# Optimization experiments

Measured on AMD Instinct MI355X. Metric: run time of the kernel, lower is better.

The kernel has to match this reference:

```python
import jax, jax.numpy as jnp
import numpy as np

B, I, H, T = 64, 128, 256, 1024


def setup_inputs() -> dict:
    key = jax.random.key(0)
    ks = jax.random.split(key, 18)
    stdv = 1.0 / np.sqrt(H)  # reset_parameters: uniform(-1/sqrt(hidden), 1/sqrt(hidden))
    u = lambda k, shape: jax.random.uniform(k, shape, jnp.float32, -stdv, stdv)
    return dict(
        X=jax.random.normal(ks[0], (B, I, T), jnp.float32),
        Mask=jax.random.randint(ks[1], (B, I, T), 0, 2).astype(jnp.float32),
        Delta=jax.random.uniform(ks[2], (B, I, T), jnp.float32),
        x_mean=jnp.float32(0.0),
        Wdgx=u(ks[3], (I, I)), bdgx=u(ks[4], (I,)),
        Wdgh=u(ks[5], (H, I)), bdgh=u(ks[6], (H,)),
        Wxz=u(ks[7], (H, I)), Whz=u(ks[8], (H, H)), Wmz=u(ks[9], (H, I)), bmz=u(ks[10], (H,)),
        Wxr=u(ks[11], (H, I)), Whr=u(ks[12], (H, H)), Wmr=u(ks[13], (H, I)),
        Wxh=u(ks[14], (H, I)), Whh=u(ks[15], (H, H)), Wmh=u(ks[16], (H, I)), bmh=u(ks[17], (H,)),
    )


def _grud(X, Mask, Delta, x_mean, Wdgx, bdgx, Wdgh, bdgh, Wxz, Whz, Wmz, bmz,
          Wxr, Whr, Wmr, Wxh, Whh, Wmh, bmh):
    # [B, I, T] -> time-major [T, B, I] for scan
    Xt = jnp.transpose(X, (2, 0, 1))
    Mt = jnp.transpose(Mask, (2, 0, 1))
    Dt = jnp.transpose(Delta, (2, 0, 1))

    def step(carry, xs):
        h, x_last = carry            # h: [B, H], x_last: [B, I]
        x, m, d = xs                 # each [B, I]
        gamma_x = jnp.exp(-jax.nn.relu(d @ Wdgx.T + bdgx))   # [B, I]
        gamma_h = jnp.exp(-jax.nn.relu(d @ Wdgh.T + bdgh))   # [B, H]
        x_last = jnp.where(m > 0, x, x_last)
        # faithful double imputation as in the torch source
        x1 = m * x + (1 - m) * (gamma_x * x + (1 - gamma_x) * x_mean)
        x2 = m * x1 + (1 - m) * (gamma_x * x_last + (1 - gamma_x) * x_mean)
        hd = gamma_h * h
        z = jax.nn.sigmoid(x2 @ Wxz.T + hd @ Whz.T + m @ Wmz.T + bmz)
        r = jax.nn.sigmoid(x2 @ Wxr.T + hd @ Whr.T + m @ Wmr.T)
        h_tilde = jnp.tanh(x2 @ Wxh.T + (r * hd) @ Whh.T + m @ Wmh.T + bmh)
        h_new = (1 - z) * hd + z * h_tilde
        return (h_new, x_last), h_new

    h0 = jnp.zeros((X.shape[0], Whz.shape[0]), X.dtype)      # Hidden_State buffer (zeros)
    xl0 = jnp.zeros((X.shape[0], X.shape[1]), X.dtype)       # X_last_obs buffer (zeros)
    _, hs = jax.lax.scan(step, (h0, xl0), (Xt, Mt, Dt))      # hs: [T, B, H]
    return jnp.transpose(hs, (1, 0, 2))                      # [B, T, H]


def reference(X, Mask, Delta, x_mean, Wdgx, bdgx, Wdgh, bdgh, Wxz, Whz, Wmz, bmz,
              Wxr, Whr, Wmr, Wxh, Whh, Wmh, bmh):
    return _grud(X, Mask, Delta, x_mean, Wdgx, bdgx, Wdgh, bdgh, Wxz, Whz, Wmz, bmz,
                 Wxr, Whr, Wmr, Wxh, Whh, Wmh, bmh)
```

## Files before the change

### kernel.cpp

```cpp
#include <hip/hip_runtime.h>
#include <cstdint>
#include <cstddef>

typedef _Float16 f16;
typedef _Float16 f16x8 __attribute__((ext_vector_type(8)));
typedef _Float16 f16x2 __attribute__((ext_vector_type(2)));
typedef float f32x4 __attribute__((ext_vector_type(4)));

#define B_ 64
#define I_ 128
#define H_ 256
#define T_ 1024
#define BT_ (B_*T_)

__device__ __forceinline__ uint32_t pack2_f16(float a, float b) {
  union { f16 h; uint16_t u; } ua, ub;
  ua.h = (f16)a; ub.h = (f16)b;
  return ((uint32_t)ub.u << 16) | (uint32_t)ua.u;
}

__device__ __forceinline__ float fdot2_u(uint32_t w, uint32_t x, float acc) {
  union { uint32_t u; f16x2 h; } uw, ux;
  uw.u = w; ux.u = x;
  return __builtin_amdgcn_fdot2(uw.h, ux.h, acc, false);
}

__device__ __forceinline__ float tanh_stable(float s) {
  float a = fabsf(s);
  float e = __expf(-2.f * a);
  float t = (1.f - e) * __fdividef(1.f, 1.f + e);
  return s < 0.f ? -t : t;
}

__device__ __forceinline__ float sigmoidf(float s) {
  return __fdividef(1.f, 1.f + __expf(-s));
}

__device__ __forceinline__ f16x8 load_frag(const f16* row, int k0, int g4) {
  union { uint32_t u[4]; f16x8 h; } r;
  const uint32_t* p0 = (const uint32_t*)(row + k0 + g4);
  const uint32_t* p1 = (const uint32_t*)(row + k0 + 16 + g4);
  r.u[0] = p0[0]; r.u[1] = p0[1];
  r.u[2] = p1[0]; r.u[3] = p1[1];
  return r.h;
}

__global__ void k_transpose_d(const float* __restrict__ D, f16* __restrict__ Dt) {
  __shared__ float tile[64][65];
  int t0 = blockIdx.x * 64, i0 = blockIdx.y * 64, b = blockIdx.z;
  int tx = threadIdx.x, ty = threadIdx.y;
  #pragma unroll
  for (int r = 0; r < 16; ++r) {
    int il = ty + r * 4;
    tile[il][tx] = D[((size_t)(b * I_ + i0 + il)) * T_ + t0 + tx];
  }
  __syncthreads();
  #pragma unroll
  for (int r = 0; r < 16; ++r) {
    int tl = ty + r * 4;
    Dt[((size_t)(b * T_ + t0 + tl)) * I_ + i0 + tx] = (f16)tile[tx][tl];
  }
}

__global__ void k_prep(const float* __restrict__ Wdgx, const float* __restrict__ bdgx,
                       const float* __restrict__ Wdgh, const float* __restrict__ bdgh,
                       const float* __restrict__ Wxz, const float* __restrict__ Whz,
                       const float* __restrict__ Wmz, const float* __restrict__ bmz,
                       const float* __restrict__ Wxr, const float* __restrict__ Whr,
                       const float* __restrict__ Wmr,
                       const float* __restrict__ Wxh, const float* __restrict__ Whh,
                       const float* __restrict__ Wmh, const float* __restrict__ bmh,
                       f16* __restrict__ Wg, float* __restrict__ bg,
                       f16* __restrict__ W3, float* __restrict__ b3,
                       uint32_t* __restrict__ blobR, uint32_t* __restrict__ blobHrg,
                       uint32_t* __restrict__ blobZ4, uint32_t* __restrict__ blobHl4) {
  int tid = blockIdx.x * blockDim.x + threadIdx.x;
  int nth = gridDim.x * blockDim.x;
  for (int idx = tid; idx < 384 * 128; idx += nth) {
    int j = idx >> 7, k = idx & 127;
    float v = (j < 128) ? Wdgx[j * 128 + k] : Wdgh[(j - 128) * 128 + k];
    Wg[idx] = (f16)v;
  }
  for (int j = tid; j < 384; j += nth) bg[j] = (j < 128) ? bdgx[j] : bdgh[j - 128];
  for (int idx = tid; idx < 768 * 256; idx += nth) {
    int j = idx >> 8, c = idx & 255;
    const float* Wx = (j < 256) ? Wxz : ((j < 512) ? Wxr : Wxh);
    const float* Wm = (j < 256) ? Wmz : ((j < 512) ? Wmr : Wmh);
    int jj = j & 255;
    float v = (c < 128) ? Wx[jj * 128 + c] : Wm[jj * 128 + (c - 128)];
    W3[idx] = (f16)v;
  }
  for (int j = tid; j < 768; j += nth)
    b3[j] = (j < 256) ? bmz[j] : ((j < 512) ? 0.0f : bmh[j - 512]);
  for (int idx = tid; idx < 64 * 512; idx += nth) {
    int c = idx >> 9, t = idx & 511;
    int rr = c >> 5, cc = c & 31;
    int ks = t >> 7, rg = t & 127;
    int row = rg * 2 + rr;
    int k = ks * 64 + cc * 2;
    blobR[idx] = pack2_f16(Whr[row * 256 + k], Whr[row * 256 + k + 1]);
  }
  for (int idx = tid; idx < 56 * 512; idx += nth) {
    int c = idx >> 9, t = idx & 511;
    int rr = (c >= 28) ? 1 : 0, cc = c - rr * 28;
    int ks = t >> 7, rg = t & 127;
    int row = rg * 2 + rr;
    int k = ks * 64 + cc * 2;
    blobHrg[idx] = pack2_f16(Whh[row * 256 + k], Whh[row * 256 + k + 1]);
  }
  for (int idx = tid; idx < 16 * 512 * 4; idx += nth) {
    int q = idx & 3, r = idx >> 2;
    int t = r & 511, c4 = r >> 9;
    int rr = c4 >> 3, qq = c4 & 7;
    int ks = t >> 7, rg = t & 127;
    int row = rg * 2 + rr;
    int k = ks * 64 + qq * 8 + q * 2;
    blobZ4[idx] = pack2_f16(Whz[row * 256 + k], Whz[row * 256 + k + 1]);
  }
  for (int idx = tid; idx < 2 * 512 * 4; idx += nth) {
    int q = idx & 3, r = idx >> 2;
    int t = r & 511, rr = r >> 9;
    int ks = t >> 7, rg = t & 127;
    int row = rg * 2 + rr;
    int k = ks * 64 + 56 + q * 2;
    blobHl4[idx] = pack2_f16(Whh[row * 256 + k], Whh[row * 256 + k + 1]);
  }
}

__global__ __launch_bounds__(256) void k_gemm1(const f16* __restrict__ A,
                                               const f16* __restrict__ W,
                                               const float* __restrict__ bias,
                                               float* __restrict__ Gx,
                                               f16* __restrict__ Gh) {
  __shared__ __align__(16) f16 As[64][136];
  __shared__ __align__(16) f16 Ws[128][136];
  int m0 = blockIdx.x * 64, n0 = blockIdx.y * 128;
  int tid = threadIdx.x;
  {
    int r = tid >> 2, sgm = tid & 3;
    const uint4* src = (const uint4*)(A + (size_t)(m0 + r) * 128 + sgm * 32);
    uint4* dst = (uint4*)(&As[r][sgm * 32]);
    #pragma unroll
    for (int q = 0; q < 4; ++q) dst[q] = src[q];
  }
  {
    int r = tid >> 1, hf = tid & 1;
    const uint4* src = (const uint4*)(W + (size_t)(n0 + r) * 128 + hf * 64);
    uint4* dst = (uint4*)(&Ws[r][hf * 64]);
    #pragma unroll
    for (int q = 0; q < 8; ++q) dst[q] = src[q];
  }
  __syncthreads();
  int w = tid >> 6, l = tid & 63;
  int lr = l & 15, g4 = (l >> 4) * 4;
  f32x4 acc[8] = {};
  #pragma unroll
  for (int kk = 0; kk < 4; ++kk) {
    int k0 = kk * 32;
    f16x8 a = load_frag(&As[w * 16 + lr][0], k0, g4);
    #pragma unroll
    for (int nt = 0; nt < 8; ++nt) {
      f16x8 bf = load_frag(&Ws[nt * 16 + lr][0], k0, g4);
      acc[nt] = __builtin_amdgcn_mfma_f32_16x16x32_f16(a, bf, acc[nt], 0, 0, 0);
    }
  }
  int row4 = (l >> 4) * 4;
  #pragma unroll
  for (int nt = 0; nt < 8; ++nt) {
    int n = n0 + nt * 16 + lr;
    float bv = bias[n];
    #pragma unroll
    for (int reg = 0; reg < 4; ++reg) {
      int m = m0 + w * 16 + row4 + reg;
      float s = acc[nt][reg] + bv;
      float g = __expf(-fmaxf(s, 0.0f));
      if (n < 128) Gx[(size_t)m * 128 + n] = g;
      else         Gh[(size_t)m * 256 + (n - 128)] = (f16)g;
    }
  }
}

__global__ __launch_bounds__(256) void k_gemm3(const f16* __restrict__ A,
                                               const f16* __restrict__ W,
                                               const float* __restrict__ bias,
                                               f16* __restrict__ P) {
  __shared__ __align__(16) f16 As[64][136];
  __shared__ __align__(16) f16 Ws[128][136];
  int m0 = blockIdx.x * 64, n0 = blockIdx.y * 128;
  int tid = threadIdx.x;
  int w = tid >> 6, l = tid & 63, lr = l & 15, g4 = (l >> 4) * 4;
  f32x4 acc[8] = {};
  for (int kh = 0; kh < 2; ++kh) {
    {
      int r = tid >> 2, sgm = tid & 3;
      const uint4* src = (const uint4*)(A + (size_t)(m0 + r) * 256 + kh * 128 + sgm * 32);
      uint4* dst = (uint4*)(&As[r][sgm * 32]);
      #pragma unroll
      for (int q = 0; q < 4; ++q) dst[q] = src[q];
    }
    {
      int r = tid >> 1, hf = tid & 1;
      const uint4* src = (const uint4*)(W + (size_t)(n0 + r) * 256 + kh * 128 + hf * 64);
      uint4* dst = (uint4*)(&Ws[r][hf * 64]);
      #pragma unroll
      for (int q = 0; q < 8; ++q) dst[q] = src[q];
    }
    __syncthreads();
    #pragma unroll
    for (int kk = 0; kk < 4; ++kk) {
      int k0 = kk * 32;
      f16x8 a = load_frag(&As[w * 16 + lr][0], k0, g4);
      #pragma unroll
      for (int nt = 0; nt < 8; ++nt) {
        f16x8 bf = load_frag(&Ws[nt * 16 + lr][0], k0, g4);
        acc[nt] = __builtin_amdgcn_mfma_f32_16x16x32_f16(a, bf, acc[nt], 0, 0, 0);
      }
    }
    __syncthreads();
  }
  int row4 = (l >> 4) * 4;
  #pragma unroll
  for (int nt = 0; nt < 8; ++nt) {
    int n = n0 + nt * 16 + lr;
    float bv = bias[n];
    #pragma unroll
    for (int reg = 0; reg < 4; ++reg) {
      int m = m0 + w * 16 + row4 + reg;
      P[(size_t)m * 768 + n] = (f16)(acc[nt][reg] + bv);
    }
  }
}

__global__ void k_seg(const float* __restrict__ X, const float* __restrict__ M,
                      float* __restrict__ segX, float* __restrict__ segF) {
  int b = blockIdx.x, s = blockIdx.y, i = threadIdx.x;
  const float* xr = X + ((size_t)(b * I_ + i)) * T_ + s * 128;
  const float* mr = M + ((size_t)(b * I_ + i)) * T_ + s * 128;
  float last = 0.f, seen = 0.f;
  for (int t = 0; t < 128; ++t) {
    float m = mr[t];
    float x = xr[t];
    if (m > 0.f) { last = x; seen = 1.f; }
  }
  segX[((size_t)(b * I_ + i)) * 8 + s] = last;
  segF[((size_t)(b * I_ + i)) * 8 + s] = seen;
}

__global__ void k_x2(const float* __restrict__ X, const float* __restrict__ M,
                     const float* __restrict__ Gx, const float* __restrict__ xmean_p,
                     const float* __restrict__ segX, const float* __restrict__ segF,
                     f16* __restrict__ AC) {
  int b = blockIdx.x, s = blockIdx.y, i = threadIdx.x;
  float xm = xmean_p[0];
  float xl = 0.f;
  const float* sF = segF + ((size_t)(b * I_ + i)) * 8;
  const float* sX = segX + ((size_t)(b * I_ + i)) * 8;
  for (int p = 0; p < s; ++p) { if (sF[p] > 0.f) xl = sX[p]; }
  const float* xr = X + ((size_t)(b * I_ + i)) * T_;
  const float* mr = M + ((size_t)(b * I_ + i)) * T_;
  for (int tl = 0; tl < 128; ++tl) {
    int t = s * 128 + tl;
    float x = xr[t], m = mr[t];
    float gx = Gx[((size_t)(b * T_ + t)) * I_ + i];
    if (m > 0.f) xl = x;
    float x1 = m * x + (1.f - m) * (gx * x + (1.f - gx) * xm);
    float x2 = m * x1 + (1.f - m) * (gx * xl + (1.f - gx) * xm);
    size_t o = ((size_t)(b * T_ + t)) * 256;
    AC[o + i] = (f16)x2;
    AC[o + 128 + i] = (f16)m;
  }
}

__global__ __launch_bounds__(512, 2) void k_recur10(
    const f16* __restrict__ Gh, const f16* __restrict__ P,
    const uint32_t* __restrict__ blobR, const uint32_t* __restrict__ blobHrg,
    const uint32_t* __restrict__ blobZ4, const uint32_t* __restrict__ blobHl4,
    float* __restrict__ out) {
  __shared__ __align__(16) uint4 whzl[16 * 512];
  __shared__ __align__(16) uint4 whhl[2 * 512];
  __shared__ __align__(16) float partR[4][256];
  __shared__ __align__(16) float partZ[4][256];
  __shared__ __align__(16) f16 hdh[256];
  __shared__ __align__(16) f16 rhdh[256];
  int tid = threadIdx.x;
  int b = blockIdx.x;
  int ks = tid >> 7, rg = tid & 127;
  bool lo = tid < 256;

  #pragma unroll
  for (int i = 0; i < 16; ++i) whzl[i * 512 + tid] = ((const uint4*)blobZ4)[i * 512 + tid];
  #pragma unroll
  for (int i = 0; i < 2; ++i)  whhl[i * 512 + tid] = ((const uint4*)blobHl4)[i * 512 + tid];

  uint32_t wR[64], wH[56];
  #pragma unroll
  for (int c = 0; c < 64; ++c) wR[c] = blobR[c * 512 + tid];
  #pragma unroll
  for (int c = 0; c < 56; ++c) wH[c] = blobHrg[c * 512 + tid];

  const f16* gbase = Gh + (size_t)b * T_ * 256;
  const f16* pbase = P + (size_t)b * T_ * 768;
  const f16* ghp = gbase + 2 * 256 + tid;
  const f16* pzp = pbase + 768 + tid;
  const f16* php = pbase + 768 + 512 + tid;
  float* outp = out + (size_t)b * T_ * 256 + tid;

  float hd_own = 0.f, z_reg = 0.f;
  float pzr_c = (float)pbase[tid];
  float ph_c  = lo ? (float)pbase[512 + tid] : 0.f;
  float gh_u  = lo ? (float)gbase[256 + tid] : 0.f;
  if (lo) hdh[tid] = (f16)0.f;
  __syncthreads();

  for (int it = 0; it < T_; ++it) {
    {
      const uint4* hd4 = (const uint4*)hdh;
      float r0 = 0.f, r1 = 0.f, z0 = 0.f, z1 = 0.f;
      #pragma unroll
      for (int c4 = 0; c4 < 8; ++c4) {
        uint4 hv = hd4[ks * 8 + c4];
        r0 = fdot2_u(wR[c4 * 4 + 0], hv.x, r0);
        r0 = fdot2_u(wR[c4 * 4 + 1], hv.y, r0);
        r0 = fdot2_u(wR[c4 * 4 + 2], hv.z, r0);
        r0 = fdot2_u(wR[c4 * 4 + 3], hv.w, r0);
        r1 = fdot2_u(wR[32 + c4 * 4 + 0], hv.x, r1);
        r1 = fdot2_u(wR[32 + c4 * 4 + 1], hv.y, r1);
        r1 = fdot2_u(wR[32 + c4 * 4 + 2], hv.z, r1);
        r1 = fdot2_u(wR[32 + c4 * 4 + 3], hv.w, r1);
        uint4 wz0 = whzl[c4 * 512 + tid];
        z0 = fdot2_u(wz0.x, hv.x, z0);
        z0 = fdot2_u(wz0.y, hv.y, z0);
        z0 = fdot2_u(wz0.z, hv.z, z0);
        z0 = fdot2_u(wz0.w, hv.w, z0);
        uint4 wz1 = whzl[(8 + c4) * 512 + tid];
        z1 = fdot2_u(wz1.x, hv.x, z1);
        z1 = fdot2_u(wz1.y, hv.y, z1);
        z1 = fdot2_u(wz1.z, hv.z, z1);
        z1 = fdot2_u(wz1.w, hv.w, z1);
        if (c4 & 1) __builtin_amdgcn_sched_barrier(0);
      }
      partR[ks][rg * 2 + 0] = r0;
      partR[ks][rg * 2 + 1] = r1;
      partZ[ks][rg * 2 + 0] = z0;
      partZ[ks][rg * 2 + 1] = z1;
    }
    float pzr_n = 0.f, ph_n = 0.f, gh_n = 0.f;
    if (it + 1 < T_) {
      pzr_n = (float)pzp[0];
      if (lo) ph_n = (float)php[0];
    }
    if (lo && it + 2 < T_) gh_n = (float)ghp[0];
    pzp += 768; php += 768; ghp += 256;
    __syncthreads();
    if (lo) {
      z_reg = sigmoidf(pzr_c + partZ[0][tid] + partZ[1][tid] + partZ[2][tid] + partZ[3][tid]);
    } else {
      int row = tid - 256;
      float s = pzr_c + partR[0][row] + partR[1][row] + partR[2][row] + partR[3][row];
      rhdh[row] = (f16)(sigmoidf(s) * (float)hdh[row]);
    }
    __syncthreads();
    {
      const uint4* rh4 = (const uint4*)rhdh;
      float h0 = 0.f, h1 = 0.f;
      #pragma unroll
      for (int c4 = 0; c4 < 7; ++c4) {
        uint4 rv = rh4[ks * 8 + c4];
        h0 = fdot2_u(wH[c4 * 4 + 0], rv.x, h0);
        h0 = fdot2_u(wH[c4 * 4 + 1], rv.y, h0);
        h0 = fdot2_u(wH[c4 * 4 + 2], rv.z, h0);
        h0 = fdot2_u(wH[c4 * 4 + 3], rv.w, h0);
        h1 = fdot2_u(wH[28 + c4 * 4 + 0], rv.x, h1);
        h1 = fdot2_u(wH[28 + c4 * 4 + 1], rv.y, h1);
        h1 = fdot2_u(wH[28 + c4 * 4 + 2], rv.z, h1);
        h1 = fdot2_u(wH[28 + c4 * 4 + 3], rv.w, h1);
        if (c4 & 1) __builtin_amdgcn_sched_barrier(0);
      }
      {
        uint4 rv = rh4[ks * 8 + 7];
        uint4 wh0 = whhl[0 * 512 + tid];
        h0 = fdot2_u(wh0.x, rv.x, h0);
        h0 = fdot2_u(wh0.y, rv.y, h0);
        h0 = fdot2_u(wh0.z, rv.z, h0);
        h0 = fdot2_u(wh0.w, rv.w, h0);
        uint4 wh1 = whhl[1 * 512 + tid];
        h1 = fdot2_u(wh1.x, rv.x, h1);
        h1 = fdot2_u(wh1.y, rv.y, h1);
        h1 = fdot2_u(wh1.z, rv.z, h1);
        h1 = fdot2_u(wh1.w, rv.w, h1);
      }
      partR[ks][rg * 2 + 0] = h0;
      partR[ks][rg * 2 + 1] = h1;
    }
    __syncthreads();
    if (lo) {
      float s2 = ph_c + partR[0][tid] + partR[1][tid] + partR[2][tid] + partR[3][tid];
      float ht = tanh_stable(s2);
      float hnew = (1.f - z_reg) * hd_own + z_reg * ht;
      outp[0] = hnew;
      outp += 256;
      hd_own = gh_u * hnew;
      hdh[tid] = (f16)hd_own;
    }
    pzr_c = pzr_n; ph_c = ph_n; gh_u = gh_n;
    __syncthreads();
  }
}

static constexpr size_t OFF_P  = 0;
static constexpr size_t OFF_DT = 0;
static constexpr size_t OFF_GX = 100663296;
static constexpr size_t OFF_GH = OFF_GX + 33554432;
static constexpr size_t OFF_AC = OFF_GH + 33554432;
static constexpr size_t OFF_WG = OFF_AC + 33554432;
static constexpr size_t OFF_BG = OFF_WG + 98304;
static constexpr size_t OFF_W3 = OFF_BG + 1536;
static constexpr size_t OFF_B3 = OFF_W3 + 393216;
static constexpr size_t OFF_BR = OFF_B3 + 3072;
static constexpr size_t OFF_BH = OFF_BR + 131072;
static constexpr size_t OFF_BZ = OFF_BH + 114688;
static constexpr size_t OFF_BL = OFF_BZ + 131072;
static constexpr size_t OFF_SX = OFF_BL + 16384;
static constexpr size_t OFF_SF = OFF_SX + 262144;
static constexpr size_t WS_TOTAL = OFF_SF + 262144;

extern "C" void kernel_launch(void* const* d_in, const int* in_sizes, int n_in,
                              void* d_out, int out_size, void* d_ws, size_t ws_size,
                              hipStream_t stream) {
  const float* X    = (const float*)d_in[0];
  const float* Mask = (const float*)d_in[1];
  const float* Delta= (const float*)d_in[2];
  const float* xm   = (const float*)d_in[3];
  const float* Wdgx = (const float*)d_in[4];
  const float* bdgx = (const float*)d_in[5];
  const float* Wdgh = (const float*)d_in[6];
  const float* bdgh = (const float*)d_in[7];
  const float* Wxz  = (const float*)d_in[8];
  const float* Whz  = (const float*)d_in[9];
  const float* Wmz  = (const float*)d_in[10];
  const float* bmz  = (const float*)d_in[11];
  const float* Wxr  = (const float*)d_in[12];
  const float* Whr  = (const float*)d_in[13];
  const float* Wmr  = (const float*)d_in[14];
  const float* Wxh  = (const float*)d_in[15];
  const float* Whh  = (const float*)d_in[16];
  const float* Wmh  = (const float*)d_in[17];
  const float* bmh  = (const float*)d_in[18];
  float* out = (float*)d_out;
  char* ws = (char*)d_ws;
  if (ws_size < WS_TOTAL) return;

  f16*      Dt   = (f16*)(ws + OFF_DT);
  f16*      P    = (f16*)(ws + OFF_P);
  float*    Gx   = (float*)(ws + OFF_GX);
  f16*      Gh   = (f16*)(ws + OFF_GH);
  f16*      AC   = (f16*)(ws + OFF_AC);
  f16*      Wg   = (f16*)(ws + OFF_WG);
  float*    bg   = (float*)(ws + OFF_BG);
  f16*      W3   = (f16*)(ws + OFF_W3);
  float*    b3   = (float*)(ws + OFF_B3);
  uint32_t* blR  = (uint32_t*)(ws + OFF_BR);
  uint32_t* blH  = (uint32_t*)(ws + OFF_BH);
  uint32_t* blZ  = (uint32_t*)(ws + OFF_BZ);
  uint32_t* blL  = (uint32_t*)(ws + OFF_BL);
  float*    segX = (float*)(ws + OFF_SX);
  float*    segF = (float*)(ws + OFF_SF);

  k_prep<<<dim3(64), dim3(256), 0, stream>>>(Wdgx, bdgx, Wdgh, bdgh, Wxz, Whz, Wmz, bmz,
                                             Wxr, Whr, Wmr, Wxh, Whh, Wmh, bmh,
                                             Wg, bg, W3, b3, blR, blH, blZ, blL);
  k_transpose_d<<<dim3(16, 2, 64), dim3(64, 4), 0, stream>>>(Delta, Dt);
  k_gemm1<<<dim3(1024, 3), dim3(256), 0, stream>>>(Dt, Wg, bg, Gx, Gh);
  k_seg<<<dim3(64, 8), dim3(128), 0, stream>>>(X, Mask, segX, segF);
  k_x2<<<dim3(64, 8), dim3(128), 0, stream>>>(X, Mask, Gx, xm, segX, segF, AC);
  k_gemm3<<<dim3(1024, 6), dim3(256), 0, stream>>>(AC, W3, b3, P);
  k_recur10<<<dim3(64), dim3(512), 0, stream>>>(Gh, P, blR, blH, blZ, blL, out);
}
```

Before: 2.203 ms.

## Rebalance Whz matvec across recurrence phases and use LDS-only barriers

```diff
diff --git a/kernel.cpp b/kernel.cpp
--- a/kernel.cpp
+++ b/kernel.cpp
@@ -34,6 +34,14 @@
 
 __device__ __forceinline__ float sigmoidf(float s) {
   return __fdividef(1.f, 1.f + __expf(-s));
+}
+
+__device__ __forceinline__ void block_bar() {
+  __builtin_amdgcn_sched_barrier(0);
+  asm volatile("s_waitcnt lgkmcnt(0)" ::: "memory");
+  __builtin_amdgcn_sched_barrier(0);
+  __builtin_amdgcn_s_barrier();
+  __builtin_amdgcn_sched_barrier(0);
 }
 
 __device__ __forceinline__ f16x8 load_frag(const f16* row, int k0, int g4) {
@@ -271,14 +279,14 @@
   }
 }
 
-__global__ __launch_bounds__(512, 2) void k_recur10(
+__global__ __launch_bounds__(512, 2) void k_recur11(
     const f16* __restrict__ Gh, const f16* __restrict__ P,
     const uint32_t* __restrict__ blobR, const uint32_t* __restrict__ blobHrg,
     const uint32_t* __restrict__ blobZ4, const uint32_t* __restrict__ blobHl4,
     float* __restrict__ out) {
   __shared__ __align__(16) uint4 whzl[16 * 512];
   __shared__ __align__(16) uint4 whhl[2 * 512];
-  __shared__ __align__(16) float partR[4][256];
+  __shared__ __align__(16) float partRH[4][256];
   __shared__ __align__(16) float partZ[4][256];
   __shared__ __align__(16) f16 hdh[256];
   __shared__ __align__(16) f16 rhdh[256];
@@ -305,7 +313,7 @@
   const f16* php = pbase + 768 + 512 + tid;
   float* outp = out + (size_t)b * T_ * 256 + tid;
 
-  float hd_own = 0.f, z_reg = 0.f;
+  float hd_own = 0.f;
   float pzr_c = (float)pbase[tid];
   float ph_c  = lo ? (float)pbase[512 + tid] : 0.f;
   float gh_u  = lo ? (float)gbase[256 + tid] : 0.f;
@@ -313,9 +321,18 @@
   __syncthreads();
 
   for (int it = 0; it < T_; ++it) {
+    float pzr_n = 0.f, ph_n = 0.f, gh_n = 0.f;
+    if (it + 1 < T_) {
+      pzr_n = (float)pzp[0];
+      if (lo) ph_n = (float)php[0];
+    }
+    if (lo && it + 2 < T_) gh_n = (float)ghp[0];
+    pzp += 768; php += 768; ghp += 256;
+
+    float z0 = 0.f, z1 = 0.f;
     {
       const uint4* hd4 = (const uint4*)hdh;
-      float r0 = 0.f, r1 = 0.f, z0 = 0.f, z1 = 0.f;
+      float r0 = 0.f, r1 = 0.f;
       #pragma unroll
       for (int c4 = 0; c4 < 8; ++c4) {
         uint4 hv = hd4[ks * 8 + c4];
@@ -327,41 +344,33 @@
         r1 = fdot2_u(wR[32 + c4 * 4 + 1], hv.y, r1);
         r1 = fdot2_u(wR[32 + c4 * 4 + 2], hv.z, r1);
         r1 = fdot2_u(wR[32 + c4 * 4 + 3], hv.w, r1);
-        uint4 wz0 = whzl[c4 * 512 + tid];
-        z0 = fdot2_u(wz0.x, hv.x, z0);
-        z0 = fdot2_u(wz0.y, hv.y, z0);
-        z0 = fdot2_u(wz0.z, hv.z, z0);
-        z0 = fdot2_u(wz0.w, hv.w, z0);
-        uint4 wz1 = whzl[(8 + c4) * 512 + tid];
-        z1 = fdot2_u(wz1.x, hv.x, z1);
-        z1 = fdot2_u(wz1.y, hv.y, z1);
-        z1 = fdot2_u(wz1.z, hv.z, z1);
-        z1 = fdot2_u(wz1.w, hv.w, z1);
+        if (c4 < 4) {
+          uint4 wz0 = whzl[c4 * 512 + tid];
+          z0 = fdot2_u(wz0.x, hv.x, z0);
+          z0 = fdot2_u(wz0.y, hv.y, z0);
+          z0 = fdot2_u(wz0.z, hv.z, z0);
+          z0 = fdot2_u(wz0.w, hv.w, z0);
+          uint4 wz1 = whzl[(8 + c4) * 512 + tid];
+          z1 = fdot2_u(wz1.x, hv.x, z1);
+          z1 = fdot2_u(wz1.y, hv.y, z1);
+          z1 = fdot2_u(wz1.z, hv.z, z1);
+          z1 = fdot2_u(wz1.w, hv.w, z1);
+        }
         if (c4 & 1) __builtin_amdgcn_sched_barrier(0);
       }
-      partR[ks][rg * 2 + 0] = r0;
-      partR[ks][rg * 2 + 1] = r1;
-      partZ[ks][rg * 2 + 0] = z0;
-      partZ[ks][rg * 2 + 1] = z1;
-    }
-    float pzr_n = 0.f, ph_n = 0.f, gh_n = 0.f;
-    if (it + 1 < T_) {
-      pzr_n = (float)pzp[0];
-      if (lo) ph_n = (float)php[0];
-    }
-    if (lo && it + 2 < T_) gh_n = (float)ghp[0];
-    pzp += 768; php += 768; ghp += 256;
-    __syncthreads();
-    if (lo) {
-      z_reg = sigmoidf(pzr_c + partZ[0][tid] + partZ[1][tid] + partZ[2][tid] + partZ[3][tid]);
-    } else {
+      partRH[ks][rg * 2 + 0] = r0;
+      partRH[ks][rg * 2 + 1] = r1;
+    }
+    block_bar();
+    if (!lo) {
       int row = tid - 256;
-      float s = pzr_c + partR[0][row] + partR[1][row] + partR[2][row] + partR[3][row];
+      float s = pzr_c + partRH[0][row] + partRH[1][row] + partRH[2][row] + partRH[3][row];
       rhdh[row] = (f16)(sigmoidf(s) * (float)hdh[row]);
     }
-    __syncthreads();
+    block_bar();
     {
       const uint4* rh4 = (const uint4*)rhdh;
+      const uint4* hd4 = (const uint4*)hdh;
       float h0 = 0.f, h1 = 0.f;
       #pragma unroll
       for (int c4 = 0; c4 < 7; ++c4) {
@@ -374,6 +383,8 @@
         h1 = fdot2_u(wH[28 + c4 * 4 + 1], rv.y, h1);
         h1 = fdot2_u(wH[28 + c4 * 4 + 2], rv.z, h1);
         h1 = fdot2_u(wH[28 + c4 * 4 + 3], rv.w, h1);
+        if (c4 >= 4 || c4 == 3) {
+        }
         if (c4 & 1) __builtin_amdgcn_sched_barrier(0);
       }
       {
@@ -389,21 +400,40 @@
         h1 = fdot2_u(wh1.z, rv.z, h1);
         h1 = fdot2_u(wh1.w, rv.w, h1);
       }
-      partR[ks][rg * 2 + 0] = h0;
-      partR[ks][rg * 2 + 1] = h1;
-    }
-    __syncthreads();
+      #pragma unroll
+      for (int c4 = 4; c4 < 8; ++c4) {
+        uint4 hv = hd4[ks * 8 + c4];
+        uint4 wz0 = whzl[c4 * 512 + tid];
+        z0 = fdot2_u(wz0.x, hv.x, z0);
+        z0 = fdot2_u(wz0.y, hv.y, z0);
+        z0 = fdot2_u(wz0.z, hv.z, z0);
+        z0 = fdot2_u(wz0.w, hv.w, z0);
+        uint4 wz1 = whzl[(8 + c4) * 512 + tid];
+        z1 = fdot2_u(wz1.x, hv.x, z1);
+        z1 = fdot2_u(wz1.y, hv.y, z1);
+        z1 = fdot2_u(wz1.z, hv.z, z1);
+        z1 = fdot2_u(wz1.w, hv.w, z1);
+        if (c4 & 1) __builtin_amdgcn_sched_barrier(0);
+      }
+      partRH[ks][rg * 2 + 0] = h0;
+      partRH[ks][rg * 2 + 1] = h1;
+      partZ[ks][rg * 2 + 0] = z0;
+      partZ[ks][rg * 2 + 1] = z1;
+    }
+    block_bar();
     if (lo) {
-      float s2 = ph_c + partR[0][tid] + partR[1][tid] + partR[2][tid] + partR[3][tid];
+      float sz = pzr_c + partZ[0][tid] + partZ[1][tid] + partZ[2][tid] + partZ[3][tid];
+      float zz = sigmoidf(sz);
+      float s2 = ph_c + partRH[0][tid] + partRH[1][tid] + partRH[2][tid] + partRH[3][tid];
       float ht = tanh_stable(s2);
-      float hnew = (1.f - z_reg) * hd_own + z_reg * ht;
+      float hnew = (1.f - zz) * hd_own + zz * ht;
       outp[0] = hnew;
       outp += 256;
       hd_own = gh_u * hnew;
       hdh[tid] = (f16)hd_own;
     }
     pzr_c = pzr_n; ph_c = ph_n; gh_u = gh_n;
-    __syncthreads();
+    block_bar();
   }
 }
 
@@ -474,5 +504,5 @@
   k_seg<<<dim3(64, 8), dim3(128), 0, stream>>>(X, Mask, segX, segF);
   k_x2<<<dim3(64, 8), dim3(128), 0, stream>>>(X, Mask, Gx, xm, segX, segF, AC);
   k_gemm3<<<dim3(1024, 6), dim3(256), 0, stream>>>(AC, W3, b3, P);
-  k_recur10<<<dim3(64), dim3(512), 0, stream>>>(Gh, P, blR, blH, blZ, blL, out);
-}
+  k_recur11<<<dim3(64), dim3(512), 0, stream>>>(Gh, P, blR, blH, blZ, blL, out);
+}
```

Result: slower. 2.425 ms (+10.0%).

## Reduce recurrence partial sums with wave shuffles and cut barriers per step

Applied to the files above, without the earlier changes.

```diff
diff --git a/kernel.cpp b/kernel.cpp
--- a/kernel.cpp
+++ b/kernel.cpp
@@ -34,6 +34,13 @@
 
 __device__ __forceinline__ float sigmoidf(float s) {
   return __fdividef(1.f, 1.f + __expf(-s));
+}
+
+__device__ __forceinline__ void bar_lgkm() {
+  __builtin_amdgcn_sched_barrier(0);
+  asm volatile("s_waitcnt lgkmcnt(0)" ::: "memory");
+  __builtin_amdgcn_s_barrier();
+  __builtin_amdgcn_sched_barrier(0);
 }
 
 __device__ __forceinline__ f16x8 load_frag(const f16* row, int k0, int g4) {
@@ -94,34 +101,34 @@
     b3[j] = (j < 256) ? bmz[j] : ((j < 512) ? 0.0f : bmh[j - 512]);
   for (int idx = tid; idx < 64 * 512; idx += nth) {
     int c = idx >> 9, t = idx & 511;
-    int rr = c >> 5, cc = c & 31;
-    int ks = t >> 7, rg = t & 127;
-    int row = rg * 2 + rr;
+    int p = c >> 5, cc = c & 31;
+    int w = t >> 6, l = t & 63, rloc = l >> 2, ks = l & 3;
+    int row = w * 16 + rloc + p * 128;
     int k = ks * 64 + cc * 2;
     blobR[idx] = pack2_f16(Whr[row * 256 + k], Whr[row * 256 + k + 1]);
   }
   for (int idx = tid; idx < 56 * 512; idx += nth) {
     int c = idx >> 9, t = idx & 511;
-    int rr = (c >= 28) ? 1 : 0, cc = c - rr * 28;
-    int ks = t >> 7, rg = t & 127;
-    int row = rg * 2 + rr;
+    int p = (c >= 28) ? 1 : 0, cc = c - p * 28;
+    int w = t >> 6, l = t & 63, rloc = l >> 2, ks = l & 3;
+    int row = w * 16 + rloc + p * 128;
     int k = ks * 64 + cc * 2;
     blobHrg[idx] = pack2_f16(Whh[row * 256 + k], Whh[row * 256 + k + 1]);
   }
   for (int idx = tid; idx < 16 * 512 * 4; idx += nth) {
     int q = idx & 3, r = idx >> 2;
     int t = r & 511, c4 = r >> 9;
-    int rr = c4 >> 3, qq = c4 & 7;
-    int ks = t >> 7, rg = t & 127;
-    int row = rg * 2 + rr;
+    int p = c4 >> 3, qq = c4 & 7;
+    int w = t >> 6, l = t & 63, rloc = l >> 2, ks = l & 3;
+    int row = w * 16 + rloc + p * 128;
     int k = ks * 64 + qq * 8 + q * 2;
     blobZ4[idx] = pack2_f16(Whz[row * 256 + k], Whz[row * 256 + k + 1]);
   }
   for (int idx = tid; idx < 2 * 512 * 4; idx += nth) {
     int q = idx & 3, r = idx >> 2;
-    int t = r & 511, rr = r >> 9;
-    int ks = t >> 7, rg = t & 127;
-    int row = rg * 2 + rr;
+    int t = r & 511, p = r >> 9;
+    int w = t >> 6, l = t & 63, rloc = l >> 2, ks = l & 3;
+    int row = w * 16 + rloc + p * 128;
     int k = ks * 64 + 56 + q * 2;
     blobHl4[idx] = pack2_f16(Whh[row * 256 + k], Whh[row * 256 + k + 1]);
   }
@@ -271,139 +278,151 @@
   }
 }
 
-__global__ __launch_bounds__(512, 2) void k_recur10(
+__global__ __launch_bounds__(512, 2) void k_recur12(
     const f16* __restrict__ Gh, const f16* __restrict__ P,
     const uint32_t* __restrict__ blobR, const uint32_t* __restrict__ blobHrg,
     const uint32_t* __restrict__ blobZ4, const uint32_t* __restrict__ blobHl4,
     float* __restrict__ out) {
   __shared__ __align__(16) uint4 whzl[16 * 512];
   __shared__ __align__(16) uint4 whhl[2 * 512];
-  __shared__ __align__(16) float partR[4][256];
-  __shared__ __align__(16) float partZ[4][256];
   __shared__ __align__(16) f16 hdh[256];
   __shared__ __align__(16) f16 rhdh[256];
   int tid = threadIdx.x;
   int b = blockIdx.x;
-  int ks = tid >> 7, rg = tid & 127;
-  bool lo = tid < 256;
+  int w = tid >> 6, l = tid & 63;
+  int rloc = l >> 2, ks = l & 3;
+  bool upd = (ks == 0);
+  int row0 = w * 16 + rloc;
+  int row1 = row0 + 128;
 
   #pragma unroll
   for (int i = 0; i < 16; ++i) whzl[i * 512 + tid] = ((const uint4*)blobZ4)[i * 512 + tid];
   #pragma unroll
   for (int i = 0; i < 2; ++i)  whhl[i * 512 + tid] = ((const uint4*)blobHl4)[i * 512 + tid];
 
-  uint32_t wR[64], wH[56];
-  #pragma unroll
-  for (int c = 0; c < 64; ++c) wR[c] = blobR[c * 512 + tid];
-  #pragma unroll
-  for (int c = 0; c < 56; ++c) wH[c] = blobHrg[c * 512 + tid];
+  uint32_t wr[64], wh[56];
+  #pragma unroll
+  for (int c = 0; c < 64; ++c) wr[c] = blobR[c * 512 + tid];
+  #pragma unroll
+  for (int c = 0; c < 56; ++c) wh[c] = blobHrg[c * 512 + tid];
 
   const f16* gbase = Gh + (size_t)b * T_ * 256;
   const f16* pbase = P + (size_t)b * T_ * 768;
-  const f16* ghp = gbase + 2 * 256 + tid;
-  const f16* pzp = pbase + 768 + tid;
-  const f16* php = pbase + 768 + 512 + tid;
-  float* outp = out + (size_t)b * T_ * 256 + tid;
-
-  float hd_own = 0.f, z_reg = 0.f;
-  float pzr_c = (float)pbase[tid];
-  float ph_c  = lo ? (float)pbase[512 + tid] : 0.f;
-  float gh_u  = lo ? (float)gbase[256 + tid] : 0.f;
-  if (lo) hdh[tid] = (f16)0.f;
+  float* outb = out + (size_t)b * T_ * 256;
+
+  if (tid < 256) hdh[tid] = (f16)0.f;
+  float hd0 = 0.f, hd1 = 0.f;
+  float pr0 = (float)pbase[256 + row0];
+  float pr1 = (float)pbase[256 + row1];
+  float pz0 = 0.f, pz1 = 0.f, ph0 = 0.f, ph1 = 0.f, g0 = 0.f, g1 = 0.f;
+  if (upd) {
+    pz0 = (float)pbase[row0];        pz1 = (float)pbase[row1];
+    ph0 = (float)pbase[512 + row0];  ph1 = (float)pbase[512 + row1];
+    g0  = (float)gbase[256 + row0];  g1  = (float)gbase[256 + row1];
+  }
   __syncthreads();
 
   for (int it = 0; it < T_; ++it) {
+    float pr0n = 0.f, pr1n = 0.f, pz0n = 0.f, pz1n = 0.f, ph0n = 0.f, ph1n = 0.f,
+          g0n = 0.f, g1n = 0.f;
+    if (it + 1 < T_) {
+      const f16* pn = pbase + (size_t)(it + 1) * 768;
+      pr0n = (float)pn[256 + row0];
+      pr1n = (float)pn[256 + row1];
+      if (upd) {
+        pz0n = (float)pn[row0];       pz1n = (float)pn[row1];
+        ph0n = (float)pn[512 + row0]; ph1n = (float)pn[512 + row1];
+      }
+    }
+    if (upd && it + 2 < T_) {
+      const f16* gn = gbase + (size_t)(it + 2) * 256;
+      g0n = (float)gn[row0]; g1n = (float)gn[row1];
+    }
+
+    const uint4* hd4 = (const uint4*)hdh;
+    float r0a = 0.f, r0b = 0.f, r1a = 0.f, r1b = 0.f;
+    float z0a = 0.f, z0b = 0.f, z1a = 0.f, z1b = 0.f;
+    #pragma unroll
+    for (int c4 = 0; c4 < 8; ++c4) {
+      uint4 hv = hd4[ks * 8 + c4];
+      r0a = fdot2_u(wr[c4 * 4 + 0], hv.x, r0a);
+      r0b = fdot2_u(wr[c4 * 4 + 1], hv.y, r0b);
+      r0a = fdot2_u(wr[c4 * 4 + 2], hv.z, r0a);
+      r0b = fdot2_u(wr[c4 * 4 + 3], hv.w, r0b);
+      r1a = fdot2_u(wr[32 + c4 * 4 + 0], hv.x, r1a);
+      r1b = fdot2_u(wr[32 + c4 * 4 + 1], hv.y, r1b);
+      r1a = fdot2_u(wr[32 + c4 * 4 + 2], hv.z, r1a);
+      r1b = fdot2_u(wr[32 + c4 * 4 + 3], hv.w, r1b);
+      uint4 zv0 = whzl[c4 * 512 + tid];
+      z0a = fdot2_u(zv0.x, hv.x, z0a);
+      z0b = fdot2_u(zv0.y, hv.y, z0b);
+      z0a = fdot2_u(zv0.z, hv.z, z0a);
+      z0b = fdot2_u(zv0.w, hv.w, z0b);
+      uint4 zv1 = whzl[(8 + c4) * 512 + tid];
+      z1a = fdot2_u(zv1.x, hv.x, z1a);
+      z1b = fdot2_u(zv1.y, hv.y, z1b);
+      z1a = fdot2_u(zv1.z, hv.z, z1a);
+      z1b = fdot2_u(zv1.w, hv.w, z1b);
+    }
+    float racc0 = r0a + r0b, racc1 = r1a + r1b;
+    float zacc0 = z0a + z0b, zacc1 = z1a + z1b;
+    racc0 += __shfl_xor(racc0, 1); racc0 += __shfl_xor(racc0, 2);
+    racc1 += __shfl_xor(racc1, 1); racc1 += __shfl_xor(racc1, 2);
+    zacc0 += __shfl_xor(zacc0, 1); zacc0 += __shfl_xor(zacc0, 2);
+    zacc1 += __shfl_xor(zacc1, 1); zacc1 += __shfl_xor(zacc1, 2);
+    if (upd) {
+      rhdh[row0] = (f16)(sigmoidf(racc0 + pr0) * hd0);
+      rhdh[row1] = (f16)(sigmoidf(racc1 + pr1) * hd1);
+    }
+    bar_lgkm();
+    const uint4* rh4 = (const uint4*)rhdh;
+    float h0a = 0.f, h0b = 0.f, h1a = 0.f, h1b = 0.f;
+    #pragma unroll
+    for (int c4 = 0; c4 < 7; ++c4) {
+      uint4 rv = rh4[ks * 8 + c4];
+      h0a = fdot2_u(wh[c4 * 4 + 0], rv.x, h0a);
+      h0b = fdot2_u(wh[c4 * 4 + 1], rv.y, h0b);
+      h0a = fdot2_u(wh[c4 * 4 + 2], rv.z, h0a);
+      h0b = fdot2_u(wh[c4 * 4 + 3], rv.w, h0b);
+      h1a = fdot2_u(wh[28 + c4 * 4 + 0], rv.x, h1a);
+      h1b = fdot2_u(wh[28 + c4 * 4 + 1], rv.y, h1b);
+      h1a = fdot2_u(wh[28 + c4 * 4 + 2], rv.z, h1a);
+      h1b = fdot2_u(wh[28 + c4 * 4 + 3], rv.w, h1b);
+    }
     {
-      const uint4* hd4 = (const uint4*)hdh;
-      float r0 = 0.f, r1 = 0.f, z0 = 0.f, z1 = 0.f;
-      #pragma unroll
-      for (int c4 = 0; c4 < 8; ++c4) {
-        uint4 hv = hd4[ks * 8 + c4];
-        r0 = fdot2_u(wR[c4 * 4 + 0], hv.x, r0);
-        r0 = fdot2_u(wR[c4 * 4 + 1], hv.y, r0);
-        r0 = fdot2_u(wR[c4 * 4 + 2], hv.z, r0);
-        r0 = fdot2_u(wR[c4 * 4 + 3], hv.w, r0);
-        r1 = fdot2_u(wR[32 + c4 * 4 + 0], hv.x, r1);
-        r1 = fdot2_u(wR[32 + c4 * 4 + 1], hv.y, r1);
-        r1 = fdot2_u(wR[32 + c4 * 4 + 2], hv.z, r1);
-        r1 = fdot2_u(wR[32 + c4 * 4 + 3], hv.w, r1);
-        uint4 wz0 = whzl[c4 * 512 + tid];
-        z0 = fdot2_u(wz0.x, hv.x, z0);
-        z0 = fdot2_u(wz0.y, hv.y, z0);
-        z0 = fdot2_u(wz0.z, hv.z, z0);
-        z0 = fdot2_u(wz0.w, hv.w, z0);
-        uint4 wz1 = whzl[(8 + c4) * 512 + tid];
-        z1 = fdot2_u(wz1.x, hv.x, z1);
-        z1 = fdot2_u(wz1.y, hv.y, z1);
-        z1 = fdot2_u(wz1.z, hv.z, z1);
-        z1 = fdot2_u(wz1.w, hv.w, z1);
-        if (c4 & 1) __builtin_amdgcn_sched_barrier(0);
-      }
-      partR[ks][rg * 2 + 0] = r0;
-      partR[ks][rg * 2 + 1] = r1;
-      partZ[ks][rg * 2 + 0] = z0;
-      partZ[ks][rg * 2 + 1] = z1;
-    }
-    float pzr_n = 0.f, ph_n = 0.f, gh_n = 0.f;
-    if (it + 1 < T_) {
-      pzr_n = (float)pzp[0];
-      if (lo) ph_n = (float)php[0];
-    }
-    if (lo && it + 2 < T_) gh_n = (float)ghp[0];
-    pzp += 768; php += 768; ghp += 256;
-    __syncthreads();
-    if (lo) {
-      z_reg = sigmoidf(pzr_c + partZ[0][tid] + partZ[1][tid] + partZ[2][tid] + partZ[3][tid]);
-    } else {
-      int row = tid - 256;
-      float s = pzr_c + partR[0][row] + partR[1][row] + partR[2][row] + partR[3][row];
-      rhdh[row] = (f16)(sigmoidf(s) * (float)hdh[row]);
-    }
-    __syncthreads();
-    {
-      const uint4* rh4 = (const uint4*)rhdh;
-      float h0 = 0.f, h1 = 0.f;
-      #pragma unroll
-      for (int c4 = 0; c4 < 7; ++c4) {
-        uint4 rv = rh4[ks * 8 + c4];
-        h0 = fdot2_u(wH[c4 * 4 + 0], rv.x, h0);
-        h0 = fdot2_u(wH[c4 * 4 + 1], rv.y, h0);
-        h0 = fdot2_u(wH[c4 * 4 + 2], rv.z, h0);
-        h0 = fdot2_u(wH[c4 * 4 + 3], rv.w, h0);
-        h1 = fdot2_u(wH[28 + c4 * 4 + 0], rv.x, h1);
-        h1 = fdot2_u(wH[28 + c4 * 4 + 1], rv.y, h1);
-        h1 = fdot2_u(wH[28 + c4 * 4 + 2], rv.z, h1);
-        h1 = fdot2_u(wH[28 + c4 * 4 + 3], rv.w, h1);
-        if (c4 & 1) __builtin_amdgcn_sched_barrier(0);
-      }
-      {
-        uint4 rv = rh4[ks * 8 + 7];
-        uint4 wh0 = whhl[0 * 512 + tid];
-        h0 = fdot2_u(wh0.x, rv.x, h0);
-        h0 = fdot2_u(wh0.y, rv.y, h0);
-        h0 = fdot2_u(wh0.z, rv.z, h0);
-        h0 = fdot2_u(wh0.w, rv.w, h0);
-        uint4 wh1 = whhl[1 * 512 + tid];
-        h1 = fdot2_u(wh1.x, rv.x, h1);
-        h1 = fdot2_u(wh1.y, rv.y, h1);
-        h1 = fdot2_u(wh1.z, rv.z, h1);
-        h1 = fdot2_u(wh1.w, rv.w, h1);
-      }
-      partR[ks][rg * 2 + 0] = h0;
-      partR[ks][rg * 2 + 1] = h1;
-    }
-    __syncthreads();
-    if (lo) {
-      float s2 = ph_c + partR[0][tid] + partR[1][tid] + partR[2][tid] + partR[3][tid];
-      float ht = tanh_stable(s2);
-      float hnew = (1.f - z_reg) * hd_own + z_reg * ht;
-      outp[0] = hnew;
-      outp += 256;
-      hd_own = gh_u * hnew;
-      hdh[tid] = (f16)hd_own;
-    }
-    pzr_c = pzr_n; ph_c = ph_n; gh_u = gh_n;
-    __syncthreads();
+      uint4 rv = rh4[ks * 8 + 7];
+      uint4 wv0 = whhl[0 * 512 + tid];
+      h0a = fdot2_u(wv0.x, rv.x, h0a);
+      h0b = fdot2_u(wv0.y, rv.y, h0b);
+      h0a = fdot2_u(wv0.z, rv.z, h0a);
+      h0b = fdot2_u(wv0.w, rv.w, h0b);
+      uint4 wv1 = whhl[1 * 512 + tid];
+      h1a = fdot2_u(wv1.x, rv.x, h1a);
+      h1b = fdot2_u(wv1.y, rv.y, h1b);
+      h1a = fdot2_u(wv1.z, rv.z, h1a);
+      h1b = fdot2_u(wv1.w, rv.w, h1b);
+    }
+    float hacc0 = h0a + h0b, hacc1 = h1a + h1b;
+    hacc0 += __shfl_xor(hacc0, 1); hacc0 += __shfl_xor(hacc0, 2);
+    hacc1 += __shfl_xor(hacc1, 1); hacc1 += __shfl_xor(hacc1, 2);
+    if (upd) {
+      float z0v = sigmoidf(zacc0 + pz0);
+      float z1v = sigmoidf(zacc1 + pz1);
+      float ht0 = tanh_stable(hacc0 + ph0);
+      float ht1 = tanh_stable(hacc1 + ph1);
+      float hn0 = (1.f - z0v) * hd0 + z0v * ht0;
+      float hn1 = (1.f - z1v) * hd1 + z1v * ht1;
+      float* o = outb + (size_t)it * 256;
+      o[row0] = hn0;
+      o[row1] = hn1;
+      hd0 = g0 * hn0;
+      hd1 = g1 * hn1;
+      hdh[row0] = (f16)hd0;
+      hdh[row1] = (f16)hd1;
+    }
+    pr0 = pr0n; pr1 = pr1n; pz0 = pz0n; pz1 = pz1n;
+    ph0 = ph0n; ph1 = ph1n; g0 = g0n; g1 = g1n;
+    bar_lgkm();
   }
 }
 
@@ -474,5 +493,5 @@
   k_seg<<<dim3(64, 8), dim3(128), 0, stream>>>(X, Mask, segX, segF);
   k_x2<<<dim3(64, 8), dim3(128), 0, stream>>>(X, Mask, Gx, xm, segX, segF, AC);
   k_gemm3<<<dim3(1024, 6), dim3(256), 0, stream>>>(AC, W3, b3, P);
-  k_recur10<<<dim3(64), dim3(512), 0, stream>>>(Gh, P, blR, blH, blZ, blL, out);
-}
+  k_recur12<<<dim3(64), dim3(512), 0, stream>>>(Gh, P, blR, blH, blZ, blL, out);
+}
```

New measurement: 2.822 ms. +28.1%, slower.
